# Optimization experiments

Hardware: AMD Instinct MI355X
Metric: run time of the kernel (lower is better)

## Reference

```python
import jax, jax.numpy as jnp
import numpy as np

NEG_INF = -1e30


def setup_inputs() -> dict:
    key = jax.random.key(0)
    k1, k2, k3, k4 = jax.random.split(key, 4)
    B, T, C, H = 4, 4096, 1024, 64
    x = jax.random.normal(k1, (B, T, C), dtype=jnp.float32)
    Wk = jax.random.normal(k2, (C, H), dtype=jnp.float32) * (C ** -0.5)
    Wq = jax.random.normal(k3, (C, H), dtype=jnp.float32) * (C ** -0.5)
    Wv = jax.random.normal(k4, (C, H), dtype=jnp.float32) * (C ** -0.5)
    return {"x": x, "Wk": Wk, "Wq": Wq, "Wv": Wv}


def reference(x, Wk, Wq, Wv):
    # x: [B, T, C]; Wq/Wk/Wv: [C, H]
    B, T, C = x.shape
    q = jnp.einsum('btc,ch->bth', x, Wq)  # [B,T,H]
    k = jnp.einsum('btc,ch->bth', x, Wk)  # [B,T,H]
    v = jnp.einsum('btc,ch->bth', x, Wv)  # [B,T,H]
    # NOTE: original scales by C**-0.5 (n_embd), not head_size**-0.5.
    scale = jnp.asarray(C, x.dtype) ** -0.5
    wei = jnp.einsum('bth,bsh->bts', q, k) * scale  # [B,T,T]
    causal = jnp.tril(jnp.ones((T, T), dtype=bool))
    wei = jnp.where(causal, wei, NEG_INF)
    wei = jax.nn.softmax(wei, axis=-1)
    # dropout p=0.0 -> identity
    out = jnp.einsum('bts,bsh->bth', wei, v)  # [B,T,H]
    return out
```

## Files before the change

### kernel.cpp

```cpp
#include <hip/hip_runtime.h>
#include <math.h>

typedef short bfx8 __attribute__((ext_vector_type(8)));
typedef short bfx4 __attribute__((ext_vector_type(4)));
typedef float fx4  __attribute__((ext_vector_type(4)));

__device__ __forceinline__ unsigned short f2bf(float f) {
    unsigned int u = __builtin_bit_cast(unsigned int, f);
    u += 0x7FFFu + ((u >> 16) & 1u);
    return (unsigned short)(u >> 16);
}
__device__ __forceinline__ float bf2f(unsigned short s) {
    unsigned int u = ((unsigned int)s) << 16;
    return __builtin_bit_cast(float, u);
}

__global__ __launch_bounds__(256) void wt_prep(const float* __restrict__ Wq,
                                               const float* __restrict__ Wk,
                                               const float* __restrict__ Wv,
                                               unsigned short* __restrict__ wt)
{
    const int k0  = blockIdx.x * 64;
    const int mat = blockIdx.y;
    const float* W = (mat == 0) ? Wq : ((mat == 1) ? Wk : Wv);
    const float scale = (mat == 0) ? (0.03125f * 1.4426950408889634f) : 1.0f;
    __shared__ unsigned short Ls[64 * 68];
    const int t = threadIdx.x;
    #pragma unroll
    for (int i = 0; i < 4; ++i) {
        int idx4 = t + 256 * i;
        int r = idx4 >> 4, c4 = idx4 & 15;
        float4 v = *(const float4*)&W[(size_t)(k0 + r) * 64 + c4 * 4];
        Ls[r * 68 + c4 * 4 + 0] = f2bf(v.x * scale);
        Ls[r * 68 + c4 * 4 + 1] = f2bf(v.y * scale);
        Ls[r * 68 + c4 * 4 + 2] = f2bf(v.z * scale);
        Ls[r * 68 + c4 * 4 + 3] = f2bf(v.w * scale);
    }
    __syncthreads();
    #pragma unroll
    for (int i = 0; i < 2; ++i) {
        int u = t + 256 * i;
        int n = u >> 3, kc = u & 7;
        bfx8 o;
        #pragma unroll
        for (int j = 0; j < 8; ++j) o[j] = (short)Ls[(kc * 8 + j) * 68 + n];
        *(bfx8*)&wt[(size_t)(mat * 64 + n) * 1024 + k0 + kc * 8] = o;
    }
}

__global__ __launch_bounds__(256) void qkv_mfma(
    const float* __restrict__ x, const unsigned short* __restrict__ wt,
    unsigned short* __restrict__ qb, unsigned short* __restrict__ kb,
    unsigned short* __restrict__ vt)
{
    __shared__ alignas(16) char smem[57344];
    const int t = threadIdx.x;
    const int w = t >> 6, l = t & 63, g = l >> 4, li = l & 15;
    const int m0 = blockIdx.x * 32;
    const int rh  = (w & 1) * 16;
    const int nb0 = (w >> 1) * 6;

    fx4 acc[6];
    #pragma unroll
    for (int i = 0; i < 6; ++i) acc[i] = (fx4){0.f, 0.f, 0.f, 0.f};

    float4 xr[2]; bfx8 wr[6];

#define QKV_LOAD(K0) do { \
    _Pragma("unroll") for (int i_ = 0; i_ < 2; ++i_) { int idx4 = t + 256 * i_; int r_ = idx4 >> 4, c4 = idx4 & 15; \
        xr[i_] = *(const float4*)&x[(size_t)(m0 + r_) * 1024 + (K0) + c4 * 4]; } \
    _Pragma("unroll") for (int i_ = 0; i_ < 6; ++i_) { int idx = t + 256 * i_; int n_ = idx >> 3, c_ = idx & 7; \
        wr[i_] = *(const bfx8*)&wt[(size_t)n_ * 1024 + (K0) + c_ * 8]; } \
} while (0)

#define QKV_STORE(BI) do { \
    char* xb_ = smem + (BI) * 4096; \
    char* wb_ = smem + 8192 + (BI) * 24576; \
    _Pragma("unroll") for (int i_ = 0; i_ < 2; ++i_) { int idx4 = t + 256 * i_; int r_ = idx4 >> 4, c4 = idx4 & 15; \
        bfx4 o_; o_[0] = (short)f2bf(xr[i_].x); o_[1] = (short)f2bf(xr[i_].y); \
        o_[2] = (short)f2bf(xr[i_].z); o_[3] = (short)f2bf(xr[i_].w); \
        *(bfx4*)(xb_ + ((r_ * 128 + c4 * 8) ^ ((r_ & 7) << 4))) = o_; } \
    _Pragma("unroll") for (int i_ = 0; i_ < 6; ++i_) { int idx = t + 256 * i_; int n_ = idx >> 3, c_ = idx & 7; \
        *(bfx8*)(wb_ + ((n_ * 128 + c_ * 16) ^ ((n_ & 7) << 4))) = wr[i_]; } \
} while (0)

    QKV_LOAD(0); QKV_STORE(0);
    __syncthreads();

    for (int ch = 0; ch < 16; ++ch) {
        if (ch + 1 < 16) QKV_LOAD((ch + 1) * 64);
        if (ch) __syncthreads();
        char* xb = smem + (ch & 1) * 4096;
        char* wb = smem + 8192 + (ch & 1) * 24576;
        const int arow = rh + li;
        #pragma unroll
        for (int kk = 0; kk < 2; ++kk) {
            bfx8 af = *(bfx8*)(xb + ((arow * 128 + kk * 64 + g * 16) ^ ((arow & 7) << 4)));
            #pragma unroll
            for (int nb = 0; nb < 6; ++nb) {
                int nrow = (nb0 + nb) * 16 + li;
                bfx8 bf = *(bfx8*)(wb + ((nrow * 128 + kk * 64 + g * 16) ^ ((nrow & 7) << 4)));
                acc[nb] = __builtin_amdgcn_mfma_f32_16x16x32_bf16(af, bf, acc[nb], 0, 0, 0);
            }
        }
        if (ch + 1 < 16) QKV_STORE((ch + 1) & 1);
    }

    const int mrow = m0 + rh + g * 4;
    #pragma unroll
    for (int nb = 0; nb < 6; ++nb) {
        const int nbg = nb0 + nb;
        if (nbg < 4) {
            #pragma unroll
            for (int r = 0; r < 4; ++r)
                qb[(size_t)(mrow + r) * 64 + nbg * 16 + li] = f2bf(acc[nb][r]);
        } else if (nbg < 8) {
            #pragma unroll
            for (int r = 0; r < 4; ++r)
                kb[(size_t)(mrow + r) * 64 + (nbg - 4) * 16 + li] = f2bf(acc[nb][r]);
        }
    }

    __syncthreads();
    unsigned short* Vt = (unsigned short*)smem;
    #pragma unroll
    for (int nb = 0; nb < 6; ++nb) {
        const int nbg = nb0 + nb;
        if (nbg >= 8) {
            #pragma unroll
            for (int r = 0; r < 4; ++r)
                Vt[((nbg - 8) * 16 + li) * 40 + rh + g * 4 + r] = f2bf(acc[nb][r]);
        }
    }
    __syncthreads();
    const int bb = m0 >> 12, mt = m0 & 4095;
    {
        int d = t >> 2, c = t & 3;
        *(bfx8*)&vt[((size_t)(bb * 64 + d)) * 4096 + mt + c * 8] = *(bfx8*)&Vt[d * 40 + c * 8];
    }
}

__global__ __launch_bounds__(256) void attn_mfma(
    const unsigned short* __restrict__ qb, const unsigned short* __restrict__ kb,
    const unsigned short* __restrict__ vt,
    unsigned short* __restrict__ pO, float* __restrict__ pml)
{
    __shared__ alignas(16) char smem[73728];
    const int t = threadIdx.x;
    const int w = t >> 6, l = t & 63, g = l >> 4, li = l & 15;
    const int bx = blockIdx.x;

    int b, qt, seg, kvb, nch;
    if (bx < 384) {
        int j = bx >> 2; b = bx & 3;
        if (j < 48)      { seg = 0; qt = 16 + j; }
        else if (j < 80) { seg = 1; qt = 32 + (j - 48); }
        else             { seg = 2; qt = 48 + (j - 80); }
        kvb = seg * 1024; nch = 8;
    } else {
        int j = (bx - 384) >> 2; b = bx & 3;
        qt = 63 - j; seg = qt >> 4; kvb = seg * 1024;
        nch = ((qt & 15) + 2) >> 1;
    }
    const int qbase = qt * 64;
    const int qsub = w & 1, par = w >> 1;
    const int qmax_w = qbase + qsub * 32 + 31;

    const int gg = qt >> 4, rr_ = qt & 15;
    const int slot = b * 160 + (8 * gg * (gg - 1) + rr_ * gg + qt) + seg;

    const unsigned short* Qg = qb + (size_t)b * 4096 * 64;
    const unsigned short* Kg = kb + (size_t)b * 4096 * 64;
    const unsigned short* Vg = vt + (size_t)b * 64 * 4096;

    bfx8 krg[4], vrg[4];

#define ATT_LOAD(CB) do { \
    _Pragma("unroll") for (int i_ = 0; i_ < 4; ++i_) { int idx = t + 256 * i_; int r_ = idx >> 3, c_ = idx & 7; \
        krg[i_] = *(const bfx8*)&Kg[(size_t)((CB) + r_) * 64 + c_ * 8]; } \
    _Pragma("unroll") for (int i_ = 0; i_ < 4; ++i_) { int idx = t + 256 * i_; int d_ = idx >> 4, c_ = idx & 15; \
        vrg[i_] = *(const bfx8*)&Vg[(size_t)d_ * 4096 + (CB) + c_ * 8]; } \
} while (0)

#define ATT_STORE(BI) do { \
    char* kb_ = smem + 8192  + (BI) * 16384; \
    char* vb_ = smem + 40960 + (BI) * 16384; \
    _Pragma("unroll") for (int i_ = 0; i_ < 4; ++i_) { int idx = t + 256 * i_; int r_ = idx >> 3, c_ = idx & 7; \
        *(bfx8*)(kb_ + ((r_ * 128 + c_ * 16) ^ ((r_ & 7) << 4))) = krg[i_]; } \
    _Pragma("unroll") for (int i_ = 0; i_ < 4; ++i_) { int idx = t + 256 * i_; int d_ = idx >> 4, c_ = idx & 15; \
        *(bfx8*)(vb_ + ((d_ * 256 + c_ * 16) ^ ((d_ & 7) << 4))) = vrg[i_]; } \
} while (0)

    {
        #pragma unroll
        for (int i = 0; i < 2; ++i) {
            int idx = t + 256 * i;
            int r2 = idx >> 3, c2 = idx & 7;
            bfx8 qv = *(const bfx8*)&Qg[(size_t)(qbase + r2) * 64 + c2 * 8];
            *(bfx8*)(smem + ((r2 * 128 + c2 * 16) ^ ((r2 & 7) << 4))) = qv;
        }
    }
    ATT_LOAD(kvb); ATT_STORE(0);
    __syncthreads();

    bfx8 qf[2][2];
    #pragma unroll
    for (int f = 0; f < 2; ++f) {
        const int qrow = qsub * 32 + f * 16 + li;
        const int sw = (qrow & 7) << 4;
        qf[f][0] = *(bfx8*)(smem + ((qrow * 128 + g * 16) ^ sw));
        qf[f][1] = *(bfx8*)(smem + ((qrow * 128 + 64 + g * 16) ^ sw));
    }

    fx4 o[4][2];
    #pragma unroll
    for (int i = 0; i < 4; ++i)
        #pragma unroll
        for (int f = 0; f < 2; ++f) o[i][f] = (fx4){0.f, 0.f, 0.f, 0.f};
    float lsum[2] = {0.f, 0.f};

    for (int ch = 0; ch < nch; ++ch) {
        const int cb = kvb + (ch << 7);
        if (ch + 1 < nch) ATT_LOAD(cb + 128);
        char* ks = smem + 8192  + ((ch & 1) ? 16384 : 0);
        char* vs = smem + 40960 + ((ch & 1) ? 16384 : 0);
        const int sub = cb + par * 64;
        if (sub <= qmax_w) {
            fx4 s[4][2];
            #pragma unroll
            for (int st = 0; st < 4; ++st)
                #pragma unroll
                for (int f = 0; f < 2; ++f) s[st][f] = (fx4){0.f, 0.f, 0.f, 0.f};
            __builtin_amdgcn_s_setprio(1);
            #pragma unroll
            for (int st = 0; st < 4; ++st) {
                const int krow = par * 64 + st * 16 + li;
                const int sw = (krow & 7) << 4;
                bfx8 kf0 = *(bfx8*)(ks + ((krow * 128 + g * 16) ^ sw));
                bfx8 kf1 = *(bfx8*)(ks + ((krow * 128 + 64 + g * 16) ^ sw));
                #pragma unroll
                for (int f = 0; f < 2; ++f) {
                    s[st][f] = __builtin_amdgcn_mfma_f32_16x16x32_bf16(kf0, qf[f][0], s[st][f], 0, 0, 0);
                    s[st][f] = __builtin_amdgcn_mfma_f32_16x16x32_bf16(kf1, qf[f][1], s[st][f], 0, 0, 0);
                }
            }
            __builtin_amdgcn_s_setprio(0);

            bfx8 pf0[2], pf1[2];
            #pragma unroll
            for (int f = 0; f < 2; ++f) {
                const int qmin_f = qbase + qsub * 32 + f * 16;
                float p[16];
                if (sub + 63 > qmin_f) {
                    #pragma unroll
                    for (int st = 0; st < 4; ++st)
                        #pragma unroll
                        for (int rr = 0; rr < 4; ++rr) {
                            int kv = sub + st * 16 + 4 * g + rr;
                            p[st * 4 + rr] = (kv <= qmin_f + li) ? s[st][f][rr] : -1e30f;
                        }
                } else {
                    #pragma unroll
                    for (int st = 0; st < 4; ++st)
                        #pragma unroll
                        for (int rr = 0; rr < 4; ++rr) p[st * 4 + rr] = s[st][f][rr];
                }
                #pragma unroll
                for (int e = 0; e < 16; ++e) p[e] = exp2f(p[e]);
                lsum[f] += (((p[0]+p[1])+(p[2]+p[3])) + ((p[4]+p[5])+(p[6]+p[7])))
                         + (((p[8]+p[9])+(p[10]+p[11])) + ((p[12]+p[13])+(p[14]+p[15])));
                #pragma unroll
                for (int e = 0; e < 8; ++e) {
                    pf0[f][e] = (short)f2bf(p[e]);
                    pf1[f][e] = (short)f2bf(p[8 + e]);
                }
            }

            __builtin_amdgcn_s_setprio(1);
            #pragma unroll
            for (int dblk = 0; dblk < 4; ++dblk) {
                const int dr = dblk * 16 + li;
                const int base = dr * 256 + par * 128;
                const int sw = (dr & 7) << 4;
                bfx4 a0 = *(bfx4*)(vs + ((base + 8 * g)      ^ sw));
                bfx4 a1 = *(bfx4*)(vs + ((base + 32 + 8 * g) ^ sw));
                bfx8 vf0;
                vf0[0] = a0[0]; vf0[1] = a0[1]; vf0[2] = a0[2]; vf0[3] = a0[3];
                vf0[4] = a1[0]; vf0[5] = a1[1]; vf0[6] = a1[2]; vf0[7] = a1[3];
                bfx4 b0 = *(bfx4*)(vs + ((base + 64 + 8 * g) ^ sw));
                bfx4 b1 = *(bfx4*)(vs + ((base + 96 + 8 * g) ^ sw));
                bfx8 vf1;
                vf1[0] = b0[0]; vf1[1] = b0[1]; vf1[2] = b0[2]; vf1[3] = b0[3];
                vf1[4] = b1[0]; vf1[5] = b1[1]; vf1[6] = b1[2]; vf1[7] = b1[3];
                #pragma unroll
                for (int f = 0; f < 2; ++f) {
                    o[dblk][f] = __builtin_amdgcn_mfma_f32_16x16x32_bf16(vf0, pf0[f], o[dblk][f], 0, 0, 0);
                    o[dblk][f] = __builtin_amdgcn_mfma_f32_16x16x32_bf16(vf1, pf1[f], o[dblk][f], 0, 0, 0);
                }
            }
            __builtin_amdgcn_s_setprio(0);
        }
        if (ch + 1 < nch) ATT_STORE((ch + 1) & 1);
        __syncthreads();
    }

    float* Osh = (float*)smem;
    float* lsh = (float*)(smem + 32768);
    #pragma unroll
    for (int dblk = 0; dblk < 4; ++dblk)
        #pragma unroll
        for (int f = 0; f < 2; ++f)
            #pragma unroll
            for (int r = 0; r < 4; ++r)
                Osh[(w * 32 + f * 16 + li) * 64 + dblk * 16 + g * 4 + r] = o[dblk][f][r];
    #pragma unroll
    for (int f = 0; f < 2; ++f)
        lsh[((w * 2 + f) * 4 + g) * 16 + li] = lsum[f];
    __syncthreads();

    {
        const int q = t >> 2, dg = t & 3;
        const int A = q >> 5, Bw = A + 2, fq = (q >> 4) & 1, liq = q & 15, row32 = q & 31;
        const float L =
            lsh[((A  * 2 + fq) * 4 + 0) * 16 + liq] + lsh[((A  * 2 + fq) * 4 + 1) * 16 + liq]
          + lsh[((A  * 2 + fq) * 4 + 2) * 16 + liq] + lsh[((A  * 2 + fq) * 4 + 3) * 16 + liq]
          + lsh[((Bw * 2 + fq) * 4 + 0) * 16 + liq] + lsh[((Bw * 2 + fq) * 4 + 1) * 16 + liq]
          + lsh[((Bw * 2 + fq) * 4 + 2) * 16 + liq] + lsh[((Bw * 2 + fq) * 4 + 3) * 16 + liq];
        const float* OA = &Osh[(A * 32 + row32) * 64 + dg * 16];
        const float* OB = &Osh[(Bw * 32 + row32) * 64 + dg * 16];
        bfx8 o1_, o2_;
        #pragma unroll
        for (int j = 0; j < 8; ++j) o1_[j] = (short)f2bf(OA[j] + OB[j]);
        #pragma unroll
        for (int j = 0; j < 8; ++j) o2_[j] = (short)f2bf(OA[8 + j] + OB[8 + j]);
        unsigned short* dst = pO + (size_t)slot * 4096 + q * 64 + dg * 16;
        *(bfx8*)&dst[0] = o1_;
        *(bfx8*)&dst[8] = o2_;
        if (dg == 0) pml[(size_t)slot * 64 + q] = L;
    }
}

__global__ __launch_bounds__(256) void attn_merge(
    const unsigned short* __restrict__ pO, const float* __restrict__ pml,
    float* __restrict__ out)
{
    const int b = blockIdx.x & 3, qt = blockIdx.x >> 2;
    const int gg = qt >> 4, rr = qt & 15;
    const int nseg = gg + 1;
    const int slot0 = b * 160 + (8 * gg * (gg - 1) + rr * gg + qt);
    const int t = threadIdx.x;
    const int q = t >> 2, dg = t & 3;

    float L = 0.f;
    float acc[16];
    #pragma unroll
    for (int j = 0; j < 16; ++j) acc[j] = 0.f;
    #pragma unroll
    for (int s = 0; s < 4; ++s) {
        if (s < nseg) {
            L += pml[(size_t)(slot0 + s) * 64 + q];
            const unsigned short* src = pO + (size_t)(slot0 + s) * 4096 + q * 64 + dg * 16;
            bfx8 v0 = *(const bfx8*)&src[0];
            bfx8 v1 = *(const bfx8*)&src[8];
            #pragma unroll
            for (int j = 0; j < 8; ++j) acc[j]     += bf2f((unsigned short)v0[j]);
            #pragma unroll
            for (int j = 0; j < 8; ++j) acc[8 + j] += bf2f((unsigned short)v1[j]);
        }
    }
    const float inv = 1.f / L;
    float* orow = out + ((size_t)b * 4096 + qt * 64 + q) * 64 + dg * 16;
    #pragma unroll
    for (int v4 = 0; v4 < 4; ++v4) {
        float4 r;
        r.x = acc[v4 * 4 + 0] * inv; r.y = acc[v4 * 4 + 1] * inv;
        r.z = acc[v4 * 4 + 2] * inv; r.w = acc[v4 * 4 + 3] * inv;
        *(float4*)&orow[v4 * 4] = r;
    }
}

extern "C" void kernel_launch(void* const* d_in, const int* in_sizes, int n_in,
                              void* d_out, int out_size, void* d_ws, size_t ws_size,
                              hipStream_t stream)
{
    const float* x  = (const float*)d_in[0];
    const float* Wk = (const float*)d_in[1];
    const float* Wq = (const float*)d_in[2];
    const float* Wv = (const float*)d_in[3];
    float* outp = (float*)d_out;

    char* ws = (char*)d_ws;
    unsigned short* qbuf = (unsigned short*)(ws);
    unsigned short* kbuf = (unsigned short*)(ws + 2*1024*1024);
    unsigned short* vtb  = (unsigned short*)(ws + 4*1024*1024);
    unsigned short* wtb  = (unsigned short*)(ws + 6*1024*1024);
    unsigned short* pO   = (unsigned short*)(ws + 7*1024*1024);
    float*          pml  = (float*)(ws + 12*1024*1024 + 65536);

    wt_prep<<<dim3(16, 3), 256, 0, stream>>>(Wq, Wk, Wv, wtb);
    qkv_mfma<<<512, 256, 0, stream>>>(x, wtb, qbuf, kbuf, vtb);
    attn_mfma<<<640, 256, 0, stream>>>(qbuf, kbuf, vtb, pO, pml);
    attn_merge<<<256, 256, 0, stream>>>(pO, pml, outp);
}
```

Measured before the change: 64.46 us.

## Split attention KV into 512-wide segments with 64-row chunks and smaller LDS

Re-partitions the causal attention work so each block handles a 512-key segment (up to 8 segments per query tile) in 64-key chunks instead of 1024-key segments in 128-key chunks. The grid grows to 1152 blocks, LDS per block shrinks, launch bounds request 4 blocks per CU, and Q fragments load straight from global memory. The V-transpose layout in the QKV kernel changes so the PV MFMA can read a contiguous bfx8 fragment. The goal is better load balance and occupancy. The cost is more partial outputs for the merge kernel to read and sum.

```diff
diff --git a/kernel.cpp b/kernel.cpp
--- a/kernel.cpp
+++ b/kernel.cpp
@@ -129,7 +129,7 @@
         if (nbg >= 8) {
             #pragma unroll
             for (int r = 0; r < 4; ++r)
-                Vt[((nbg - 8) * 16 + li) * 40 + rh + g * 4 + r] = f2bf(acc[nb][r]);
+                Vt[((nbg - 8) * 16 + li) * 40 + g * 8 + (rh >> 2) + r] = f2bf(acc[nb][r]);
         }
     }
     __syncthreads();
@@ -140,77 +140,71 @@
     }
 }
 
-__global__ __launch_bounds__(256) void attn_mfma(
+__global__ __launch_bounds__(256, 4) void attn_mfma(
     const unsigned short* __restrict__ qb, const unsigned short* __restrict__ kb,
     const unsigned short* __restrict__ vt,
     unsigned short* __restrict__ pO, float* __restrict__ pml)
 {
-    __shared__ alignas(16) char smem[73728];
+    __shared__ alignas(16) char smem[34816];
     const int t = threadIdx.x;
     const int w = t >> 6, l = t & 63, g = l >> 4, li = l & 15;
     const int bx = blockIdx.x;
 
-    int b, qt, seg, kvb, nch;
-    if (bx < 384) {
-        int j = bx >> 2; b = bx & 3;
-        if (j < 48)      { seg = 0; qt = 16 + j; }
-        else if (j < 80) { seg = 1; qt = 32 + (j - 48); }
-        else             { seg = 2; qt = 48 + (j - 80); }
-        kvb = seg * 1024; nch = 8;
+    const int b = bx & 3;
+    const int j = bx >> 2;
+    int qt, seg, nch;
+    if (j < 224) {
+        int a = 1;
+        #pragma unroll
+        for (int aa = 2; aa <= 7; ++aa) if (j >= 4 * aa * (aa - 1)) a = aa;
+        const int local = j - 4 * a * (a - 1);
+        qt = 8 * a + local / a;
+        seg = local % a;
+        nch = 8;
     } else {
-        int j = (bx - 384) >> 2; b = bx & 3;
-        qt = 63 - j; seg = qt >> 4; kvb = seg * 1024;
-        nch = ((qt & 15) + 2) >> 1;
+        const int jd = j - 224;
+        const int r = 7 - (jd >> 3);
+        const int a = jd & 7;
+        qt = 8 * a + r; seg = a; nch = r + 1;
     }
     const int qbase = qt * 64;
+    const int kvb = seg * 512;
     const int qsub = w & 1, par = w >> 1;
     const int qmax_w = qbase + qsub * 32 + 31;
-
-    const int gg = qt >> 4, rr_ = qt & 15;
-    const int slot = b * 160 + (8 * gg * (gg - 1) + rr_ * gg + qt) + seg;
+    const int aq = qt >> 3, rq = qt & 7;
+    const int slot = b * 288 + (aq + 1) * (4 * aq + rq) + seg;
 
     const unsigned short* Qg = qb + (size_t)b * 4096 * 64;
     const unsigned short* Kg = kb + (size_t)b * 4096 * 64;
     const unsigned short* Vg = vt + (size_t)b * 64 * 4096;
 
-    bfx8 krg[4], vrg[4];
+    bfx8 krg[2], vrg[2];
 
 #define ATT_LOAD(CB) do { \
-    _Pragma("unroll") for (int i_ = 0; i_ < 4; ++i_) { int idx = t + 256 * i_; int r_ = idx >> 3, c_ = idx & 7; \
+    _Pragma("unroll") for (int i_ = 0; i_ < 2; ++i_) { int idx = t + 256 * i_; int r_ = idx >> 3, c_ = idx & 7; \
         krg[i_] = *(const bfx8*)&Kg[(size_t)((CB) + r_) * 64 + c_ * 8]; } \
-    _Pragma("unroll") for (int i_ = 0; i_ < 4; ++i_) { int idx = t + 256 * i_; int d_ = idx >> 4, c_ = idx & 15; \
+    _Pragma("unroll") for (int i_ = 0; i_ < 2; ++i_) { int idx = t + 256 * i_; int d_ = idx >> 3, c_ = idx & 7; \
         vrg[i_] = *(const bfx8*)&Vg[(size_t)d_ * 4096 + (CB) + c_ * 8]; } \
 } while (0)
 
 #define ATT_STORE(BI) do { \
-    char* kb_ = smem + 8192  + (BI) * 16384; \
-    char* vb_ = smem + 40960 + (BI) * 16384; \
-    _Pragma("unroll") for (int i_ = 0; i_ < 4; ++i_) { int idx = t + 256 * i_; int r_ = idx >> 3, c_ = idx & 7; \
+    char* kb_ = smem + (BI) * 8192; \
+    char* vb_ = smem + 16384 + (BI) * 8192; \
+    _Pragma("unroll") for (int i_ = 0; i_ < 2; ++i_) { int idx = t + 256 * i_; int r_ = idx >> 3, c_ = idx & 7; \
         *(bfx8*)(kb_ + ((r_ * 128 + c_ * 16) ^ ((r_ & 7) << 4))) = krg[i_]; } \
-    _Pragma("unroll") for (int i_ = 0; i_ < 4; ++i_) { int idx = t + 256 * i_; int d_ = idx >> 4, c_ = idx & 15; \
-        *(bfx8*)(vb_ + ((d_ * 256 + c_ * 16) ^ ((d_ & 7) << 4))) = vrg[i_]; } \
+    _Pragma("unroll") for (int i_ = 0; i_ < 2; ++i_) { int idx = t + 256 * i_; int d_ = idx >> 3, c_ = idx & 7; \
+        *(bfx8*)(vb_ + ((d_ * 128 + c_ * 16) ^ ((d_ & 7) << 4))) = vrg[i_]; } \
 } while (0)
 
-    {
-        #pragma unroll
-        for (int i = 0; i < 2; ++i) {
-            int idx = t + 256 * i;
-            int r2 = idx >> 3, c2 = idx & 7;
-            bfx8 qv = *(const bfx8*)&Qg[(size_t)(qbase + r2) * 64 + c2 * 8];
-            *(bfx8*)(smem + ((r2 * 128 + c2 * 16) ^ ((r2 & 7) << 4))) = qv;
-        }
-    }
+    bfx8 qf[2][2];
+    #pragma unroll
+    for (int f = 0; f < 2; ++f)
+        #pragma unroll
+        for (int h = 0; h < 2; ++h)
+            qf[f][h] = *(const bfx8*)&Qg[(size_t)(qbase + qsub * 32 + f * 16 + li) * 64 + h * 32 + g * 8];
+
     ATT_LOAD(kvb); ATT_STORE(0);
     __syncthreads();
-
-    bfx8 qf[2][2];
-    #pragma unroll
-    for (int f = 0; f < 2; ++f) {
-        const int qrow = qsub * 32 + f * 16 + li;
-        const int sw = (qrow & 7) << 4;
-        qf[f][0] = *(bfx8*)(smem + ((qrow * 128 + g * 16) ^ sw));
-        qf[f][1] = *(bfx8*)(smem + ((qrow * 128 + 64 + g * 16) ^ sw));
-    }
 
     fx4 o[4][2];
     #pragma unroll
@@ -220,21 +214,21 @@
     float lsum[2] = {0.f, 0.f};
 
     for (int ch = 0; ch < nch; ++ch) {
-        const int cb = kvb + (ch << 7);
-        if (ch + 1 < nch) ATT_LOAD(cb + 128);
-        char* ks = smem + 8192  + ((ch & 1) ? 16384 : 0);
-        char* vs = smem + 40960 + ((ch & 1) ? 16384 : 0);
-        const int sub = cb + par * 64;
+        const int cb = kvb + (ch << 6);
+        if (ch + 1 < nch) ATT_LOAD(cb + 64);
+        char* ks = smem + (ch & 1) * 8192;
+        char* vs = smem + 16384 + (ch & 1) * 8192;
+        const int sub = cb + par * 32;
         if (sub <= qmax_w) {
-            fx4 s[4][2];
-            #pragma unroll
-            for (int st = 0; st < 4; ++st)
+            fx4 s[2][2];
+            #pragma unroll
+            for (int st = 0; st < 2; ++st)
                 #pragma unroll
                 for (int f = 0; f < 2; ++f) s[st][f] = (fx4){0.f, 0.f, 0.f, 0.f};
             __builtin_amdgcn_s_setprio(1);
             #pragma unroll
-            for (int st = 0; st < 4; ++st) {
-                const int krow = par * 64 + st * 16 + li;
+            for (int st = 0; st < 2; ++st) {
+                const int krow = par * 32 + st * 16 + li;
                 const int sw = (krow & 7) << 4;
                 bfx8 kf0 = *(bfx8*)(ks + ((krow * 128 + g * 16) ^ sw));
                 bfx8 kf1 = *(bfx8*)(ks + ((krow * 128 + 64 + g * 16) ^ sw));
@@ -246,14 +240,14 @@
             }
             __builtin_amdgcn_s_setprio(0);
 
-            bfx8 pf0[2], pf1[2];
+            bfx8 pf[2];
             #pragma unroll
             for (int f = 0; f < 2; ++f) {
                 const int qmin_f = qbase + qsub * 32 + f * 16;
-                float p[16];
-                if (sub + 63 > qmin_f) {
+                float p[8];
+                if (sub + 31 > qmin_f) {
                     #pragma unroll
-                    for (int st = 0; st < 4; ++st)
+                    for (int st = 0; st < 2; ++st)
                         #pragma unroll
                         for (int rr = 0; rr < 4; ++rr) {
                             int kv = sub + st * 16 + 4 * g + rr;
@@ -261,42 +255,25 @@
                         }
                 } else {
                     #pragma unroll
-                    for (int st = 0; st < 4; ++st)
+                    for (int st = 0; st < 2; ++st)
                         #pragma unroll
                         for (int rr = 0; rr < 4; ++rr) p[st * 4 + rr] = s[st][f][rr];
                 }
                 #pragma unroll
-                for (int e = 0; e < 16; ++e) p[e] = exp2f(p[e]);
-                lsum[f] += (((p[0]+p[1])+(p[2]+p[3])) + ((p[4]+p[5])+(p[6]+p[7])))
-                         + (((p[8]+p[9])+(p[10]+p[11])) + ((p[12]+p[13])+(p[14]+p[15])));
-                #pragma unroll
-                for (int e = 0; e < 8; ++e) {
-                    pf0[f][e] = (short)f2bf(p[e]);
-                    pf1[f][e] = (short)f2bf(p[8 + e]);
-                }
+                for (int e = 0; e < 8; ++e) p[e] = exp2f(p[e]);
+                lsum[f] += ((p[0]+p[1])+(p[2]+p[3])) + ((p[4]+p[5])+(p[6]+p[7]));
+                #pragma unroll
+                for (int e = 0; e < 8; ++e) pf[f][e] = (short)f2bf(p[e]);
             }
 
             __builtin_amdgcn_s_setprio(1);
             #pragma unroll
             for (int dblk = 0; dblk < 4; ++dblk) {
                 const int dr = dblk * 16 + li;
-                const int base = dr * 256 + par * 128;
-                const int sw = (dr & 7) << 4;
-                bfx4 a0 = *(bfx4*)(vs + ((base + 8 * g)      ^ sw));
-                bfx4 a1 = *(bfx4*)(vs + ((base + 32 + 8 * g) ^ sw));
-                bfx8 vf0;
-                vf0[0] = a0[0]; vf0[1] = a0[1]; vf0[2] = a0[2]; vf0[3] = a0[3];
-                vf0[4] = a1[0]; vf0[5] = a1[1]; vf0[6] = a1[2]; vf0[7] = a1[3];
-                bfx4 b0 = *(bfx4*)(vs + ((base + 64 + 8 * g) ^ sw));
-                bfx4 b1 = *(bfx4*)(vs + ((base + 96 + 8 * g) ^ sw));
-                bfx8 vf1;
-                vf1[0] = b0[0]; vf1[1] = b0[1]; vf1[2] = b0[2]; vf1[3] = b0[3];
-                vf1[4] = b1[0]; vf1[5] = b1[1]; vf1[6] = b1[2]; vf1[7] = b1[3];
-                #pragma unroll
-                for (int f = 0; f < 2; ++f) {
-                    o[dblk][f] = __builtin_amdgcn_mfma_f32_16x16x32_bf16(vf0, pf0[f], o[dblk][f], 0, 0, 0);
-                    o[dblk][f] = __builtin_amdgcn_mfma_f32_16x16x32_bf16(vf1, pf1[f], o[dblk][f], 0, 0, 0);
-                }
+                bfx8 vf = *(bfx8*)(vs + ((dr * 128 + par * 64 + g * 16) ^ ((dr & 7) << 4)));
+                #pragma unroll
+                for (int f = 0; f < 2; ++f)
+                    o[dblk][f] = __builtin_amdgcn_mfma_f32_16x16x32_bf16(vf, pf[f], o[dblk][f], 0, 0, 0);
             }
             __builtin_amdgcn_s_setprio(0);
         }
@@ -312,7 +289,7 @@
         for (int f = 0; f < 2; ++f)
             #pragma unroll
             for (int r = 0; r < 4; ++r)
-                Osh[(w * 32 + f * 16 + li) * 64 + dblk * 16 + g * 4 + r] = o[dblk][f][r];
+                Osh[(par * 64 + qsub * 32 + f * 16 + li) * 64 + dblk * 16 + g * 4 + r] = o[dblk][f][r];
     #pragma unroll
     for (int f = 0; f < 2; ++f)
         lsh[((w * 2 + f) * 4 + g) * 16 + li] = lsum[f];
@@ -320,19 +297,18 @@
 
     {
         const int q = t >> 2, dg = t & 3;
-        const int A = q >> 5, Bw = A + 2, fq = (q >> 4) & 1, liq = q & 15, row32 = q & 31;
-        const float L =
-            lsh[((A  * 2 + fq) * 4 + 0) * 16 + liq] + lsh[((A  * 2 + fq) * 4 + 1) * 16 + liq]
-          + lsh[((A  * 2 + fq) * 4 + 2) * 16 + liq] + lsh[((A  * 2 + fq) * 4 + 3) * 16 + liq]
-          + lsh[((Bw * 2 + fq) * 4 + 0) * 16 + liq] + lsh[((Bw * 2 + fq) * 4 + 1) * 16 + liq]
-          + lsh[((Bw * 2 + fq) * 4 + 2) * 16 + liq] + lsh[((Bw * 2 + fq) * 4 + 3) * 16 + liq];
-        const float* OA = &Osh[(A * 32 + row32) * 64 + dg * 16];
-        const float* OB = &Osh[(Bw * 32 + row32) * 64 + dg * 16];
+        const int A = (q >> 5), Bw = A + 2, fq = (q >> 4) & 1, liq = q & 15;
+        float L = 0.f;
+        #pragma unroll
+        for (int gg2 = 0; gg2 < 4; ++gg2)
+            L += lsh[((A * 2 + fq) * 4 + gg2) * 16 + liq] + lsh[((Bw * 2 + fq) * 4 + gg2) * 16 + liq];
+        const float* OA = &Osh[q * 64 + dg * 16];
+        const float* OB = &Osh[(64 + q) * 64 + dg * 16];
         bfx8 o1_, o2_;
         #pragma unroll
-        for (int j = 0; j < 8; ++j) o1_[j] = (short)f2bf(OA[j] + OB[j]);
-        #pragma unroll
-        for (int j = 0; j < 8; ++j) o2_[j] = (short)f2bf(OA[8 + j] + OB[8 + j]);
+        for (int jj = 0; jj < 8; ++jj) o1_[jj] = (short)f2bf(OA[jj] + OB[jj]);
+        #pragma unroll
+        for (int jj = 0; jj < 8; ++jj) o2_[jj] = (short)f2bf(OA[8 + jj] + OB[8 + jj]);
         unsigned short* dst = pO + (size_t)slot * 4096 + q * 64 + dg * 16;
         *(bfx8*)&dst[0] = o1_;
         *(bfx8*)&dst[8] = o2_;
@@ -345,37 +321,37 @@
     float* __restrict__ out)
 {
     const int b = blockIdx.x & 3, qt = blockIdx.x >> 2;
-    const int gg = qt >> 4, rr = qt & 15;
-    const int nseg = gg + 1;
-    const int slot0 = b * 160 + (8 * gg * (gg - 1) + rr * gg + qt);
+    const int a = qt >> 3, r = qt & 7;
+    const int nseg = a + 1;
+    const int slot0 = b * 288 + (a + 1) * (4 * a + r);
     const int t = threadIdx.x;
     const int q = t >> 2, dg = t & 3;
 
     float L = 0.f;
     float acc[16];
     #pragma unroll
-    for (int j = 0; j < 16; ++j) acc[j] = 0.f;
-    #pragma unroll
-    for (int s = 0; s < 4; ++s) {
+    for (int jj = 0; jj < 16; ++jj) acc[jj] = 0.f;
+    #pragma unroll
+    for (int s = 0; s < 8; ++s) {
         if (s < nseg) {
             L += pml[(size_t)(slot0 + s) * 64 + q];
             const unsigned short* src = pO + (size_t)(slot0 + s) * 4096 + q * 64 + dg * 16;
             bfx8 v0 = *(const bfx8*)&src[0];
             bfx8 v1 = *(const bfx8*)&src[8];
             #pragma unroll
-            for (int j = 0; j < 8; ++j) acc[j]     += bf2f((unsigned short)v0[j]);
-            #pragma unroll
-            for (int j = 0; j < 8; ++j) acc[8 + j] += bf2f((unsigned short)v1[j]);
+            for (int jj = 0; jj < 8; ++jj) acc[jj]     += bf2f((unsigned short)v0[jj]);
+            #pragma unroll
+            for (int jj = 0; jj < 8; ++jj) acc[8 + jj] += bf2f((unsigned short)v1[jj]);
         }
     }
     const float inv = 1.f / L;
     float* orow = out + ((size_t)b * 4096 + qt * 64 + q) * 64 + dg * 16;
     #pragma unroll
     for (int v4 = 0; v4 < 4; ++v4) {
-        float4 r;
-        r.x = acc[v4 * 4 + 0] * inv; r.y = acc[v4 * 4 + 1] * inv;
-        r.z = acc[v4 * 4 + 2] * inv; r.w = acc[v4 * 4 + 3] * inv;
-        *(float4*)&orow[v4 * 4] = r;
+        float4 rr;
+        rr.x = acc[v4 * 4 + 0] * inv; rr.y = acc[v4 * 4 + 1] * inv;
+        rr.z = acc[v4 * 4 + 2] * inv; rr.w = acc[v4 * 4 + 3] * inv;
+        *(float4*)&orow[v4 * 4] = rr;
     }
 }
 
@@ -395,10 +371,10 @@
     unsigned short* vtb  = (unsigned short*)(ws + 4*1024*1024);
     unsigned short* wtb  = (unsigned short*)(ws + 6*1024*1024);
     unsigned short* pO   = (unsigned short*)(ws + 7*1024*1024);
-    float*          pml  = (float*)(ws + 12*1024*1024 + 65536);
+    float*          pml  = (float*)(ws + 16*1024*1024 + 512*1024);
 
     wt_prep<<<dim3(16, 3), 256, 0, stream>>>(Wq, Wk, Wv, wtb);
     qkv_mfma<<<512, 256, 0, stream>>>(x, wtb, qbuf, kbuf, vtb);
-    attn_mfma<<<640, 256, 0, stream>>>(qbuf, kbuf, vtb, pO, pml);
+    attn_mfma<<<1152, 256, 0, stream>>>(qbuf, kbuf, vtb, pO, pml);
     attn_merge<<<256, 256, 0, stream>>>(pO, pml, outp);
 }
```

After: 57.33 us. -11.1%, faster.
